# Optimization experiments

Hardware: AMD Instinct MI355X
Metric: run time of the kernel (lower is better)

## Reference

```python
import jax, jax.numpy as jnp
import numpy as np

N = 50000      # nodes
E = 800000     # edges per meta-path
P = 3          # meta-paths
IN = 128       # in_size
OUT = 64       # out_size per head
H = 4          # heads
HID = 128      # semantic-attention hidden
NEG_SLOPE = 0.2


def setup_inputs() -> dict:
    key = jax.random.key(0)
    ks = jax.random.split(key, 8)
    h = jax.random.normal(ks[0], (N, IN), jnp.float32)
    edges = jax.random.randint(ks[1], (P, 2, E), 0, N, dtype=jnp.int32)  # [P, (src,dst), E]
    fc_w = jax.random.normal(ks[2], (P, IN, H * OUT), jnp.float32) * 0.05
    attn_l = jax.random.normal(ks[3], (P, H, OUT), jnp.float32) * 0.05
    attn_r = jax.random.normal(ks[4], (P, H, OUT), jnp.float32) * 0.05
    w1 = jax.random.normal(ks[5], (H * OUT, HID), jnp.float32) * 0.05
    b1 = jnp.zeros((HID,), jnp.float32)
    w2 = jax.random.normal(ks[6], (HID,), jnp.float32) * 0.05
    return {"h": h, "edges": edges, "fc_w": fc_w, "attn_l": attn_l,
            "attn_r": attn_r, "w1": w1, "b1": b1, "w2": w2}


def _gat(h, edge, fc_w, al, ar):
    # One GATConv (DGL semantics, eval mode: dropout off, no residual/bias).
    src, dst = edge[0], edge[1]
    feat = (h @ fc_w).reshape(N, H, OUT)                 # [N,H,D]
    el = jnp.einsum('nhd,hd->nh', feat, al)              # [N,H]
    er = jnp.einsum('nhd,hd->nh', feat, ar)
    e = jax.nn.leaky_relu(el[src] + er[dst], NEG_SLOPE)  # [E,H]
    # edge softmax over incoming edges of each dst node
    m = jax.ops.segment_max(e, dst, num_segments=N)      # [N,H]
    m = jnp.where(jnp.isfinite(m), m, 0.0)               # empty segments -> 0
    ex = jnp.exp(e - m[dst])
    s = jax.ops.segment_sum(ex, dst, num_segments=N)     # [N,H]
    alpha = ex / s[dst]                                  # [E,H]
    msg = feat[src] * alpha[:, :, None]                  # [E,H,D]
    rst = jax.ops.segment_sum(msg, dst, num_segments=N)  # [N,H,D]
    return jax.nn.elu(rst).reshape(N, H * OUT)


def reference(h, edges, fc_w, attn_l, attn_r, w1, b1, w2):
    # per-meta-path GAT embeddings -> [N, P, H*OUT]
    z = jnp.stack([_gat(h, edges[i], fc_w[i], attn_l[i], attn_r[i])
                   for i in range(P)], axis=1)
    # semantic attention: Linear -> tanh -> Linear(no bias) -> softmax over P
    w = jnp.tanh(z @ w1 + b1) @ w2                       # [N,P]
    beta = jax.nn.softmax(w, axis=1)[:, :, None]         # [N,P,1]
    return (beta * z).sum(axis=1)                        # [N, H*OUT]
```

## Files before the change

kernel.cpp:

```cpp
#include <hip/hip_runtime.h>
#include <hip/hip_bf16.h>
#include <hip/hip_fp16.h>

#define N_NODES 50000
#define N_EDGES 800000
#define N_PATHS 3
#define IN_F    128
#define HO      256
#define N_HEADS 4
#define HID     128

#define BLK_PER_PATH 80
#define EDGES_PER_HB 10000
#define HIST_BLOCKS  (N_PATHS * BLK_PER_PATH)
#define PREP_BLOCKS  512
#define NPACK        12500
#define FEAT_RB      782
#define SCAT_BLOCKS  2344
#define FEAT_ELEMS   ((size_t)N_NODES * HO)

typedef __bf16 bf16;
typedef __bf16 bf16x8 __attribute__((ext_vector_type(8)));
typedef float  f32x4  __attribute__((ext_vector_type(4)));
typedef unsigned short u16;
typedef unsigned char  u8;
typedef unsigned int   u32;

__device__ __forceinline__ void prep_role(int b, const float* __restrict__ fc_w,
                                          const float* __restrict__ w1,
                                          bf16* __restrict__ fcwT,
                                          bf16* __restrict__ w1T) {
    int g = b * 256 + threadIdx.x;
    if (g < N_PATHS * IN_F * HO) {
        int p = g >> 15, r = g & 32767;
        int col = r & 255, k = r >> 8;
        fcwT[(size_t)p * 32768 + col * IN_F + k] = (bf16)fc_w[(size_t)p * 32768 + k * HO + col];
    } else {
        int gg = g - N_PATHS * IN_F * HO;
        if (gg < HO * HID) {
            int k = gg & 255, j = gg >> 8;
            w1T[(size_t)j * HO + k] = (bf16)w1[(size_t)k * HID + j];
        }
    }
}

__device__ __forceinline__ void hist_role(int b, const int* __restrict__ edges,
                                          u32* __restrict__ cnt32, u8* __restrict__ lrank,
                                          u32* hist) {
    const int p = b / BLK_PER_PATH, blk = b - p * BLK_PER_PATH;
    const int t = threadIdx.x;
    for (int i = t; i < NPACK; i += 256) hist[i] = 0;
    __syncthreads();

    const int* dstp = edges + (size_t)p * 2 * N_EDGES + N_EDGES + blk * EDGES_PER_HB;
    u8* lr = lrank + (size_t)p * N_EDGES + blk * EDGES_PER_HB;
    for (int q = t; q < EDGES_PER_HB / 4; q += 256) {
        int4 d4 = ((const int4*)dstp)[q];
        u32 o0 = atomicAdd(&hist[d4.x >> 2], 1u << ((d4.x & 3) * 8));
        u32 o1 = atomicAdd(&hist[d4.y >> 2], 1u << ((d4.y & 3) * 8));
        u32 o2 = atomicAdd(&hist[d4.z >> 2], 1u << ((d4.z & 3) * 8));
        u32 o3 = atomicAdd(&hist[d4.w >> 2], 1u << ((d4.w & 3) * 8));
        uchar4 r4;
        r4.x = (u8)(o0 >> ((d4.x & 3) * 8));
        r4.y = (u8)(o1 >> ((d4.y & 3) * 8));
        r4.z = (u8)(o2 >> ((d4.z & 3) * 8));
        r4.w = (u8)(o3 >> ((d4.w & 3) * 8));
        ((uchar4*)lr)[q] = r4;
    }
    __syncthreads();
    u32* out = cnt32 + (size_t)b * NPACK;
    for (int i = t; i < NPACK; i += 256) out[i] = hist[i];
}

__global__ __launch_bounds__(256) void k_ph(const float* __restrict__ fc_w,
                                            const float* __restrict__ w1,
                                            bf16* __restrict__ fcwT,
                                            bf16* __restrict__ w1T,
                                            const int* __restrict__ edges,
                                            u32* __restrict__ cnt32,
                                            u8* __restrict__ lrank) {
    __shared__ u32 hist[NPACK];
    const int bid = blockIdx.x;
    if (bid < PREP_BLOCKS)
        prep_role(bid, fc_w, w1, fcwT, w1T);
    else
        hist_role(bid - PREP_BLOCKS, edges, cnt32, lrank, hist);
}

__global__ __launch_bounds__(256) void k_base(u32* __restrict__ cnt32,
                                              int* __restrict__ deg) {
    int g = blockIdx.x * 256 + threadIdx.x;
    if (g >= N_PATHS * NPACK) return;
    int p = g / NPACK, q = g - p * NPACK;
    u32 s0 = 0, s1 = 0, s2 = 0, s3 = 0;
#pragma unroll 8
    for (int blk = 0; blk < BLK_PER_PATH; ++blk) {
        size_t idx = (size_t)(p * BLK_PER_PATH + blk) * NPACK + q;
        u32 c = cnt32[idx];
        cnt32[idx] = s0 | (s1 << 8) | (s2 << 16) | (s3 << 24);
        s0 += c & 0xff; s1 += (c >> 8) & 0xff; s2 += (c >> 16) & 0xff; s3 += c >> 24;
    }
    int4 d4 = {(int)s0, (int)s1, (int)s2, (int)s3};
    *(int4*)(deg + (size_t)p * N_NODES + 4 * q) = d4;
}

__global__ __launch_bounds__(1024) void k_scan(const int* __restrict__ deg,
                                               int* __restrict__ rowptr) {
    __shared__ int part[1024];
    const int p = blockIdx.x;
    const int* dg = deg + p * N_NODES;
    int* rp = rowptr + p * (N_NODES + 1);

    const int tid = threadIdx.x;
    const int CH = (N_NODES + 1023) / 1024;
    const int start = tid * CH;
    int s = 0;
    for (int i = 0; i < CH; ++i) { int idx = start + i; if (idx < N_NODES) s += dg[idx]; }
    part[tid] = s;
    __syncthreads();
    for (int off = 1; off < 1024; off <<= 1) {
        int v = (tid >= off) ? part[tid - off] : 0;
        __syncthreads();
        part[tid] += v;
        __syncthreads();
    }
    int excl = (tid == 0) ? 0 : part[tid - 1];
    for (int i = 0; i < CH; ++i) {
        int idx = start + i;
        if (idx < N_NODES) { rp[idx] = excl; excl += dg[idx]; }
    }
    if (tid == 1023) rp[N_NODES] = N_EDGES;
}

__device__ __forceinline__ void scatter_role(int b, const int* __restrict__ edges,
                                             const u8* __restrict__ lrank,
                                             const u32* __restrict__ cnt32,
                                             const int* __restrict__ rowptr,
                                             u16* __restrict__ csrAll) {
    int gt = b * 256 + threadIdx.x;
    if (gt >= (N_PATHS * N_EDGES) / 4) return;
    int base = gt * 4;
    int p = base / N_EDGES, e = base - p * N_EDGES;
    const int blk = e / EDGES_PER_HB;
    const int* ep = edges + (size_t)p * 2 * N_EDGES;
    int4 s4 = *(const int4*)(ep + e);
    int4 d4 = *(const int4*)(ep + N_EDGES + e);
    uchar4 r4 = *(const uchar4*)(lrank + base);
    const int* rp = rowptr + p * (N_NODES + 1);
    const u32* bb = cnt32 + (size_t)(p * BLK_PER_PATH + blk) * NPACK;
    u16* c = csrAll + (size_t)p * N_EDGES;
    int p0 = rp[d4.x] + (int)((bb[d4.x >> 2] >> ((d4.x & 3) * 8)) & 0xff) + r4.x;
    int p1 = rp[d4.y] + (int)((bb[d4.y >> 2] >> ((d4.y & 3) * 8)) & 0xff) + r4.y;
    int p2 = rp[d4.z] + (int)((bb[d4.z >> 2] >> ((d4.z & 3) * 8)) & 0xff) + r4.z;
    int p3 = rp[d4.w] + (int)((bb[d4.w >> 2] >> ((d4.w & 3) * 8)) & 0xff) + r4.w;
    c[p0] = (u16)s4.x; c[p1] = (u16)s4.y; c[p2] = (u16)s4.z; c[p3] = (u16)s4.w;
}

__device__ __forceinline__ void feat_role(int rb, const float* __restrict__ h,
                                          const bf16* __restrict__ fcwT,
                                          const float* __restrict__ al,
                                          const float* __restrict__ ar,
                                          __half* __restrict__ featAll,
                                          float* __restrict__ elAll,
                                          float* __restrict__ erAll) {
    const int t = threadIdx.x, w = t >> 6, l = t & 63, lo = l & 15, hi = l >> 4;
    const int arow = rb * 64 + w * 16 + lo;
    const int crow = rb * 64 + w * 16 + hi * 4;

    bf16x8 afr[4];
    if (arow < N_NODES) {
        const float* hp = h + (size_t)arow * IN_F;
#pragma unroll
        for (int ks = 0; ks < 4; ++ks) {
            float4 f0 = *(const float4*)(hp + ks * 32 + hi * 8);
            float4 f1 = *(const float4*)(hp + ks * 32 + hi * 8 + 4);
            bf16x8 a;
            a[0]=(bf16)f0.x; a[1]=(bf16)f0.y; a[2]=(bf16)f0.z; a[3]=(bf16)f0.w;
            a[4]=(bf16)f1.x; a[5]=(bf16)f1.y; a[6]=(bf16)f1.z; a[7]=(bf16)f1.w;
            afr[ks] = a;
        }
    } else {
#pragma unroll
        for (int ks = 0; ks < 4; ++ks) { bf16x8 a = {}; afr[ks] = a; }
    }

    for (int p = 0; p < N_PATHS; ++p) {
        __half* feat = featAll + (size_t)p * FEAT_ELEMS;
        const float* alp = al + p * HO;
        const float* arp = ar + p * HO;
        float* elA = elAll + (size_t)p * N_NODES * 4;
        float* erA = erAll + (size_t)p * N_NODES * 4;
#pragma unroll
        for (int ch = 0; ch < 2; ++ch) {
            const bf16* W = fcwT + (size_t)p * 32768 + (size_t)ch * 128 * IN_F;
            f32x4 acc[8];
#pragma unroll
            for (int c = 0; c < 8; ++c) { f32x4 zz = {0.f,0.f,0.f,0.f}; acc[c] = zz; }
#pragma unroll
            for (int ctl = 0; ctl < 8; ++ctl) {
                const bf16* wp = W + (size_t)(ctl * 16 + lo) * IN_F + hi * 8;
                f32x4 a = acc[ctl];
#pragma unroll
                for (int ks = 0; ks < 4; ++ks)
                    a = __builtin_amdgcn_mfma_f32_16x16x32_bf16(afr[ks], *(const bf16x8*)(wp + ks * 32), a, 0, 0, 0);
                acc[ctl] = a;
            }
            float elP[2][4] = {{0}}, erP[2][4] = {{0}};
#pragma unroll
            for (int ctl = 0; ctl < 8; ++ctl) {
                const int gcol = ch * 128 + ctl * 16 + lo;
                const float av = alp[gcol], bv = arp[gcol];
                const int hl = ctl >> 2;
#pragma unroll
                for (int rr = 0; rr < 4; ++rr) {
                    float v = acc[ctl][rr];
                    elP[hl][rr] = fmaf(v, av, elP[hl][rr]);
                    erP[hl][rr] = fmaf(v, bv, erP[hl][rr]);
                    if (crow + rr < N_NODES)
                        feat[(size_t)(crow + rr) * HO + gcol] = __float2half(v);
                }
            }
#pragma unroll
            for (int hl = 0; hl < 2; ++hl)
#pragma unroll
                for (int rr = 0; rr < 4; ++rr) {
                    float v = elP[hl][rr], u = erP[hl][rr];
#pragma unroll
                    for (int m = 1; m <= 8; m <<= 1) {
                        v += __shfl_xor(v, m, 64);
                        u += __shfl_xor(u, m, 64);
                    }
                    elP[hl][rr] = v; erP[hl][rr] = u;
                }
            if (lo == 0) {
#pragma unroll
                for (int rr = 0; rr < 4; ++rr) {
                    if (crow + rr < N_NODES) {
                        *(float2*)&elA[(crow + rr) * 4 + ch * 2] = make_float2(elP[0][rr], elP[1][rr]);
                        *(float2*)&erA[(crow + rr) * 4 + ch * 2] = make_float2(erP[0][rr], erP[1][rr]);
                    }
                }
            }
        }
    }
}

__global__ __launch_bounds__(256) void k_sf(const int* __restrict__ edges,
                                            const u8* __restrict__ lrank,
                                            const u32* __restrict__ cnt32,
                                            const int* __restrict__ rowptr,
                                            u16* __restrict__ csr,
                                            const float* __restrict__ h,
                                            const bf16* __restrict__ fcwT,
                                            const float* __restrict__ al,
                                            const float* __restrict__ ar,
                                            __half* __restrict__ featAll,
                                            float* __restrict__ elAll,
                                            float* __restrict__ erAll) {
    const int bid = blockIdx.x;
    if (bid < SCAT_BLOCKS)
        scatter_role(bid, edges, lrank, cnt32, rowptr, csr);
    else
        feat_role(bid - SCAT_BLOCKS, h, fcwT, al, ar, featAll, elAll, erAll);
}

__global__ __launch_bounds__(256) void k_gather3(const u16* __restrict__ csrAll,
                                                 const int* __restrict__ rowptrAll,
                                                 const float4* __restrict__ elAll,
                                                 const float4* __restrict__ erAll,
                                                 const __half* __restrict__ featAll,
                                                 bf16* __restrict__ z) {
    __shared__ u32     s_off[4][64];
    __shared__ __half2 s_ad[4][4][66];
    const int pb = blockIdx.x;
    const int p  = pb / (N_NODES / 4);
    const int nb = pb - p * (N_NODES / 4);

    const int t = threadIdx.x, w = t >> 6, l = t & 63;
    const int half = l >> 5, c = l & 31, hh = c >> 3;
    const int n = nb * 4 + w;

    const u16*    csr    = csrAll + (size_t)p * N_EDGES;
    const int*    rowptr = rowptrAll + p * (N_NODES + 1);
    const float4* el4    = elAll + (size_t)p * N_NODES;
    const __half* feat   = featAll + (size_t)p * FEAT_ELEMS;

    const int b0 = rowptr[n], b1e = rowptr[n + 1];
    const float4 er_n = (erAll + (size_t)p * N_NODES)[n];

    __half2 acc0 = __float2half2_rn(0.f), acc1 = acc0, acc2 = acc0, acc3 = acc0;
    float4 den = {0.f, 0.f, 0.f, 0.f};

    for (int base = b0; base < b1e; base += 64) {
        const int cnt = min(64, b1e - base);
        if (l < cnt) {
            int sv = csr[base + l];
            s_off[w][l] = (u32)(sv * HO);
            float4 e = el4[sv];
            float vx = e.x + er_n.x, vy = e.y + er_n.y,
                  vz = e.z + er_n.z, vw = e.w + er_n.w;
            vx = (vx >= 0.f) ? vx : 0.2f * vx;
            vy = (vy >= 0.f) ? vy : 0.2f * vy;
            vz = (vz >= 0.f) ? vz : 0.2f * vz;
            vw = (vw >= 0.f) ? vw : 0.2f * vw;
            float ex = __expf(vx), ey = __expf(vy), ez = __expf(vz), ew = __expf(vw);
            den.x += ex; den.y += ey; den.z += ez; den.w += ew;
            s_ad[w][0][l] = __float2half2_rn(ex);
            s_ad[w][1][l] = __float2half2_rn(ey);
            s_ad[w][2][l] = __float2half2_rn(ez);
            s_ad[w][3][l] = __float2half2_rn(ew);
        }
        int i2 = 0;
        for (; i2 + 8 <= cnt; i2 += 8) {
            const int e0 = i2 + half, e1 = i2 + 2 + half,
                      e2 = i2 + 4 + half, e3 = i2 + 6 + half;
            u32 o0 = s_off[w][e0], o1 = s_off[w][e1], o2 = s_off[w][e2], o3 = s_off[w][e3];
            __half2 a0 = s_ad[w][hh][e0], a1 = s_ad[w][hh][e1],
                    a2 = s_ad[w][hh][e2], a3 = s_ad[w][hh][e3];
            const uint4 u0 = *(const uint4*)(feat + o0 + c * 8);
            const uint4 u1 = *(const uint4*)(feat + o1 + c * 8);
            const uint4 u2 = *(const uint4*)(feat + o2 + c * 8);
            const uint4 u3 = *(const uint4*)(feat + o3 + c * 8);
            acc0 = __hfma2(__builtin_bit_cast(__half2, u0.x), a0, acc0);
            acc1 = __hfma2(__builtin_bit_cast(__half2, u0.y), a0, acc1);
            acc2 = __hfma2(__builtin_bit_cast(__half2, u0.z), a0, acc2);
            acc3 = __hfma2(__builtin_bit_cast(__half2, u0.w), a0, acc3);
            acc0 = __hfma2(__builtin_bit_cast(__half2, u1.x), a1, acc0);
            acc1 = __hfma2(__builtin_bit_cast(__half2, u1.y), a1, acc1);
            acc2 = __hfma2(__builtin_bit_cast(__half2, u1.z), a1, acc2);
            acc3 = __hfma2(__builtin_bit_cast(__half2, u1.w), a1, acc3);
            acc0 = __hfma2(__builtin_bit_cast(__half2, u2.x), a2, acc0);
            acc1 = __hfma2(__builtin_bit_cast(__half2, u2.y), a2, acc1);
            acc2 = __hfma2(__builtin_bit_cast(__half2, u2.z), a2, acc2);
            acc3 = __hfma2(__builtin_bit_cast(__half2, u2.w), a2, acc3);
            acc0 = __hfma2(__builtin_bit_cast(__half2, u3.x), a3, acc0);
            acc1 = __hfma2(__builtin_bit_cast(__half2, u3.y), a3, acc1);
            acc2 = __hfma2(__builtin_bit_cast(__half2, u3.z), a3, acc2);
            acc3 = __hfma2(__builtin_bit_cast(__half2, u3.w), a3, acc3);
        }
        for (; i2 + 4 <= cnt; i2 += 4) {
            const int e0 = i2 + half, e1 = i2 + 2 + half;
            u32 o0 = s_off[w][e0], o1 = s_off[w][e1];
            __half2 a0 = s_ad[w][hh][e0], a1 = s_ad[w][hh][e1];
            const uint4 u0 = *(const uint4*)(feat + o0 + c * 8);
            const uint4 u1 = *(const uint4*)(feat + o1 + c * 8);
            acc0 = __hfma2(__builtin_bit_cast(__half2, u0.x), a0, acc0);
            acc1 = __hfma2(__builtin_bit_cast(__half2, u0.y), a0, acc1);
            acc2 = __hfma2(__builtin_bit_cast(__half2, u0.z), a0, acc2);
            acc3 = __hfma2(__builtin_bit_cast(__half2, u0.w), a0, acc3);
            acc0 = __hfma2(__builtin_bit_cast(__half2, u1.x), a1, acc0);
            acc1 = __hfma2(__builtin_bit_cast(__half2, u1.y), a1, acc1);
            acc2 = __hfma2(__builtin_bit_cast(__half2, u1.z), a1, acc2);
            acc3 = __hfma2(__builtin_bit_cast(__half2, u1.w), a1, acc3);
        }
        for (; i2 < cnt; i2 += 2) {
            const int e = i2 + half;
            if (e < cnt) {
                u32 o0 = s_off[w][e];
                __half2 a0 = s_ad[w][hh][e];
                const uint4 u = *(const uint4*)(feat + o0 + c * 8);
                acc0 = __hfma2(__builtin_bit_cast(__half2, u.x), a0, acc0);
                acc1 = __hfma2(__builtin_bit_cast(__half2, u.y), a0, acc1);
                acc2 = __hfma2(__builtin_bit_cast(__half2, u.z), a0, acc2);
                acc3 = __hfma2(__builtin_bit_cast(__half2, u.w), a0, acc3);
            }
        }
    }

    float s[8];
    { float2 f0 = __half22float2(acc0), f1 = __half22float2(acc1),
             f2 = __half22float2(acc2), f3 = __half22float2(acc3);
      s[0]=f0.x; s[1]=f0.y; s[2]=f1.x; s[3]=f1.y; s[4]=f2.x; s[5]=f2.y; s[6]=f3.x; s[7]=f3.y; }
#pragma unroll
    for (int j = 0; j < 8; ++j) s[j] += __shfl_xor(s[j], 32, 64);
#pragma unroll
    for (int off = 32; off; off >>= 1) {
        den.x += __shfl_xor(den.x, off, 64);
        den.y += __shfl_xor(den.y, off, 64);
        den.z += __shfl_xor(den.z, off, 64);
        den.w += __shfl_xor(den.w, off, 64);
    }
    const float d = (hh == 0) ? den.x : (hh == 1) ? den.y : (hh == 2) ? den.z : den.w;
    const float inv = (d > 0.f) ? 1.f / d : 0.f;
    if (half == 0) {
        bf16x8 ov;
#pragma unroll
        for (int j = 0; j < 8; ++j) {
            float v = s[j] * inv;
            v = (v > 0.f) ? v : expm1f(v);
            ov[j] = (bf16)v;
        }
        *(bf16x8*)(z + (size_t)n * (N_PATHS * HO) + p * HO + c * 8) = ov;
    }
}

__global__ __launch_bounds__(256) void k_semout(const bf16* __restrict__ z,
                                                const bf16* __restrict__ w1T,
                                                const float* __restrict__ b1,
                                                const float* __restrict__ w2,
                                                float* __restrict__ out) {
    __shared__ bf16  zs[48 * 264];
    __shared__ float psem[4][48];
    __shared__ float betas[16][4];

    const int t = threadIdx.x, w = t >> 6, l = t & 63;
    const int lo = l & 15, hi = l >> 4;
    const int n0 = blockIdx.x * 16;

    bf16x8 bfr[2][8];
#pragma unroll
    for (int ct = 0; ct < 2; ++ct) {
        const int j = (2 * w + ct) * 16 + lo;
#pragma unroll
        for (int s = 0; s < 8; ++s)
            bfr[ct][s] = *(const bf16x8*)(w1T + (size_t)j * HO + s * 32 + hi * 8);
    }

    const uint4* zg4 = (const uint4*)(z + (size_t)n0 * (N_PATHS * HO));
    for (int i = t; i < 1536; i += 256) {
        uint4 v = zg4[i];
        int r = i >> 5, cin = (i & 31) * 8;
        *(uint4*)&zs[r * 264 + cin] = v;
    }
    __syncthreads();

    f32x4 acc[2][3];
#pragma unroll
    for (int ct = 0; ct < 2; ++ct)
#pragma unroll
        for (int m = 0; m < 3; ++m) { f32x4 zz = {0.f,0.f,0.f,0.f}; acc[ct][m] = zz; }

    for (int s = 0; s < 8; ++s) {
#pragma unroll
        for (int m = 0; m < 3; ++m) {
            bf16x8 a = *(const bf16x8*)&zs[(m * 16 + lo) * 264 + s * 32 + hi * 8];
            acc[0][m] = __builtin_amdgcn_mfma_f32_16x16x32_bf16(a, bfr[0][s], acc[0][m], 0, 0, 0);
            acc[1][m] = __builtin_amdgcn_mfma_f32_16x16x32_bf16(a, bfr[1][s], acc[1][m], 0, 0, 0);
        }
    }

    const int j0 = (2 * w + 0) * 16 + lo;
    const int j1 = (2 * w + 1) * 16 + lo;
    const float b1_0 = b1[j0], w2_0 = w2[j0];
    const float b1_1 = b1[j1], w2_1 = w2[j1];
#pragma unroll
    for (int m = 0; m < 3; ++m) {
#pragma unroll
        for (int r = 0; r < 4; ++r) {
            float tt = tanhf(acc[0][m][r] + b1_0) * w2_0
                     + tanhf(acc[1][m][r] + b1_1) * w2_1;
            tt += __shfl_xor(tt, 1, 64);
            tt += __shfl_xor(tt, 2, 64);
            tt += __shfl_xor(tt, 4, 64);
            tt += __shfl_xor(tt, 8, 64);
            if (lo == 0) psem[w][m * 16 + hi * 4 + r] = tt;
        }
    }
    __syncthreads();
    if (t < 48) psem[0][t] = psem[0][t] + psem[1][t] + psem[2][t] + psem[3][t];
    __syncthreads();
    if (t < 16) {
        float a0 = psem[0][3 * t], a1 = psem[0][3 * t + 1], a2 = psem[0][3 * t + 2];
        float mx = fmaxf(a0, fmaxf(a1, a2));
        float e0 = __expf(a0 - mx), e1 = __expf(a1 - mx), e2 = __expf(a2 - mx);
        float is = 1.f / (e0 + e1 + e2);
        betas[t][0] = e0 * is; betas[t][1] = e1 * is; betas[t][2] = e2 * is;
    }
    __syncthreads();
    for (int i = 0; i < 16; ++i) {
        float bb0 = betas[i][0], bb1 = betas[i][1], bb2 = betas[i][2];
        float o = bb0 * (float)zs[(3 * i + 0) * 264 + t]
                + bb1 * (float)zs[(3 * i + 1) * 264 + t]
                + bb2 * (float)zs[(3 * i + 2) * 264 + t];
        out[(size_t)(n0 + i) * HO + t] = o;
    }
}

static inline size_t align256(size_t x) { return (x + 255) & ~(size_t)255; }

extern "C" void kernel_launch(void* const* d_in, const int* in_sizes, int n_in,
                              void* d_out, int out_size, void* d_ws, size_t ws_size,
                              hipStream_t stream) {
    const float* h     = (const float*)d_in[0];
    const int*   edges = (const int*)d_in[1];
    const float* fc_w  = (const float*)d_in[2];
    const float* al    = (const float*)d_in[3];
    const float* ar    = (const float*)d_in[4];
    const float* w1    = (const float*)d_in[5];
    const float* b1    = (const float*)d_in[6];
    const float* w2    = (const float*)d_in[7];
    float* out = (float*)d_out;

    char* base = (char*)d_ws;
    size_t off = 0;
    auto carve = [&](size_t bytes) -> char* {
        char* p = base + off; off = align256(off + bytes); return p;
    };
    __half* feat   = (__half*)carve((size_t)N_PATHS * FEAT_ELEMS * 2);
    bf16*   zbuf   = (bf16*)carve((size_t)N_NODES * N_PATHS * HO * 2);
    u16*    csr    = (u16*)carve((size_t)N_PATHS * N_EDGES * 2);
    bf16*   fcwT   = (bf16*)carve((size_t)N_PATHS * IN_F * HO * 2);
    bf16*   w1T    = (bf16*)carve((size_t)HO * HID * 2);
    float*  el     = (float*)carve((size_t)N_PATHS * N_NODES * 4 * 4);
    float*  er     = (float*)carve((size_t)N_PATHS * N_NODES * 4 * 4);
    int*    deg    = (int*)carve((size_t)N_PATHS * N_NODES * 4);
    int*    rowptr = (int*)carve((size_t)N_PATHS * (N_NODES + 1) * 4);
    u8*     lrank  = (u8*)carve((size_t)N_PATHS * N_EDGES);
    u32*    cnt32  = (u32*)carve((size_t)HIST_BLOCKS * NPACK * 4);
    (void)ws_size; (void)in_sizes; (void)n_in; (void)out_size;

    k_ph<<<PREP_BLOCKS + HIST_BLOCKS, 256, 0, stream>>>(
        fc_w, w1, fcwT, w1T, edges, cnt32, lrank);
    k_base<<<(N_PATHS * NPACK + 255) / 256, 256, 0, stream>>>(cnt32, deg);
    k_scan<<<N_PATHS, 1024, 0, stream>>>(deg, rowptr);
    k_sf<<<SCAT_BLOCKS + FEAT_RB, 256, 0, stream>>>(
        edges, lrank, cnt32, rowptr, csr, h, fcwT, al, ar, feat, el, er);
    k_gather3<<<N_PATHS * (N_NODES / 4), 256, 0, stream>>>(
        csr, rowptr, (const float4*)el, (const float4*)er, feat, zbuf);
    k_semout<<<N_NODES / 16, 256, 0, stream>>>(zbuf, w1T, b1, w2, out);
}
```

Before: 487.6 us.

## Fuse degree scan into base kernel via last-block counter; pack gather LDS entries

Removes the separate k_scan launch. The last k_base block to finish, found through an atomic counter with thread fences, now runs the prefix scan for all three paths. That scan uses a single 256-thread block instead of three 1024-thread blocks, so it runs serially across paths with longer per-thread chunks. The gather kernel also packs each edge's source offset and half2 attention weight into one uint2 in shared memory, so each edge needs one LDS read instead of two.

```diff
diff --git a/kernel.cpp b/kernel.cpp
--- a/kernel.cpp
+++ b/kernel.cpp
@@ -17,6 +17,7 @@
 #define NPACK        12500
 #define FEAT_RB      782
 #define SCAT_BLOCKS  2344
+#define BASE_BLOCKS  147
 #define FEAT_ELEMS   ((size_t)N_NODES * HO)
 
 typedef __bf16 bf16;
@@ -29,7 +30,9 @@
 __device__ __forceinline__ void prep_role(int b, const float* __restrict__ fc_w,
                                           const float* __restrict__ w1,
                                           bf16* __restrict__ fcwT,
-                                          bf16* __restrict__ w1T) {
+                                          bf16* __restrict__ w1T,
+                                          u32* __restrict__ ctr) {
+    if (b == 0 && threadIdx.x == 0) *ctr = 0;
     int g = b * 256 + threadIdx.x;
     if (g < N_PATHS * IN_F * HO) {
         int p = g >> 15, r = g & 32767;
@@ -78,58 +81,68 @@
                                             bf16* __restrict__ w1T,
                                             const int* __restrict__ edges,
                                             u32* __restrict__ cnt32,
-                                            u8* __restrict__ lrank) {
+                                            u8* __restrict__ lrank,
+                                            u32* __restrict__ ctr) {
     __shared__ u32 hist[NPACK];
     const int bid = blockIdx.x;
     if (bid < PREP_BLOCKS)
-        prep_role(bid, fc_w, w1, fcwT, w1T);
+        prep_role(bid, fc_w, w1, fcwT, w1T, ctr);
     else
         hist_role(bid - PREP_BLOCKS, edges, cnt32, lrank, hist);
 }
 
 __global__ __launch_bounds__(256) void k_base(u32* __restrict__ cnt32,
-                                              int* __restrict__ deg) {
+                                              int* __restrict__ deg,
+                                              int* __restrict__ rowptr,
+                                              u32* __restrict__ ctr) {
     int g = blockIdx.x * 256 + threadIdx.x;
-    if (g >= N_PATHS * NPACK) return;
-    int p = g / NPACK, q = g - p * NPACK;
-    u32 s0 = 0, s1 = 0, s2 = 0, s3 = 0;
+    if (g < N_PATHS * NPACK) {
+        int p = g / NPACK, q = g - p * NPACK;
+        u32 s0 = 0, s1 = 0, s2 = 0, s3 = 0;
 #pragma unroll 8
-    for (int blk = 0; blk < BLK_PER_PATH; ++blk) {
-        size_t idx = (size_t)(p * BLK_PER_PATH + blk) * NPACK + q;
-        u32 c = cnt32[idx];
-        cnt32[idx] = s0 | (s1 << 8) | (s2 << 16) | (s3 << 24);
-        s0 += c & 0xff; s1 += (c >> 8) & 0xff; s2 += (c >> 16) & 0xff; s3 += c >> 24;
-    }
-    int4 d4 = {(int)s0, (int)s1, (int)s2, (int)s3};
-    *(int4*)(deg + (size_t)p * N_NODES + 4 * q) = d4;
-}
-
-__global__ __launch_bounds__(1024) void k_scan(const int* __restrict__ deg,
-                                               int* __restrict__ rowptr) {
-    __shared__ int part[1024];
-    const int p = blockIdx.x;
-    const int* dg = deg + p * N_NODES;
-    int* rp = rowptr + p * (N_NODES + 1);
-
+        for (int blk = 0; blk < BLK_PER_PATH; ++blk) {
+            size_t idx = (size_t)(p * BLK_PER_PATH + blk) * NPACK + q;
+            u32 c = cnt32[idx];
+            cnt32[idx] = s0 | (s1 << 8) | (s2 << 16) | (s3 << 24);
+            s0 += c & 0xff; s1 += (c >> 8) & 0xff; s2 += (c >> 16) & 0xff; s3 += c >> 24;
+        }
+        int4 d4 = {(int)s0, (int)s1, (int)s2, (int)s3};
+        *(int4*)(deg + (size_t)p * N_NODES + 4 * q) = d4;
+    }
+    __syncthreads();
+    __threadfence();
+    __shared__ u32 done;
+    if (threadIdx.x == 0) done = atomicAdd(ctr, 1);
+    __syncthreads();
+    if (done != (u32)(gridDim.x - 1)) return;
+    __threadfence();
+
+    __shared__ int part[256];
     const int tid = threadIdx.x;
-    const int CH = (N_NODES + 1023) / 1024;
-    const int start = tid * CH;
-    int s = 0;
-    for (int i = 0; i < CH; ++i) { int idx = start + i; if (idx < N_NODES) s += dg[idx]; }
-    part[tid] = s;
-    __syncthreads();
-    for (int off = 1; off < 1024; off <<= 1) {
-        int v = (tid >= off) ? part[tid - off] : 0;
+    const int CH = 196;
+    for (int p = 0; p < N_PATHS; ++p) {
+        const int* dg = deg + (size_t)p * N_NODES;
+        int* rp = rowptr + p * (N_NODES + 1);
+        const int st = tid * CH;
+        int s = 0;
+        for (int i = 0; i < CH; ++i) { int idx = st + i; if (idx < N_NODES) s += dg[idx]; }
+        part[tid] = s;
         __syncthreads();
-        part[tid] += v;
+        for (int off = 1; off < 256; off <<= 1) {
+            int v = (tid >= off) ? part[tid - off] : 0;
+            __syncthreads();
+            part[tid] += v;
+            __syncthreads();
+        }
+        int excl = (tid == 0) ? 0 : part[tid - 1];
+        for (int i = 0; i < CH; ++i) {
+            int idx = st + i;
+            if (idx < N_NODES) { rp[idx] = excl; excl += dg[idx]; }
+        }
+        if (tid == 255) rp[N_NODES] = N_EDGES;
         __syncthreads();
     }
-    int excl = (tid == 0) ? 0 : part[tid - 1];
-    for (int i = 0; i < CH; ++i) {
-        int idx = start + i;
-        if (idx < N_NODES) { rp[idx] = excl; excl += dg[idx]; }
-    }
-    if (tid == 1023) rp[N_NODES] = N_EDGES;
+    if (tid == 0) *ctr = 0;
 }
 
 __device__ __forceinline__ void scatter_role(int b, const int* __restrict__ edges,
@@ -270,8 +283,7 @@
                                                  const float4* __restrict__ erAll,
                                                  const __half* __restrict__ featAll,
                                                  bf16* __restrict__ z) {
-    __shared__ u32     s_off[4][64];
-    __shared__ __half2 s_ad[4][4][66];
+    __shared__ uint2 s_pk[4][4][66];
     const int pb = blockIdx.x;
     const int p  = pb / (N_NODES / 4);
     const int nb = pb - p * (N_NODES / 4);
@@ -295,7 +307,7 @@
         const int cnt = min(64, b1e - base);
         if (l < cnt) {
             int sv = csr[base + l];
-            s_off[w][l] = (u32)(sv * HO);
+            u32 off = (u32)(sv * HO);
             float4 e = el4[sv];
             float vx = e.x + er_n.x, vy = e.y + er_n.y,
                   vz = e.z + er_n.z, vw = e.w + er_n.w;
@@ -305,22 +317,30 @@
             vw = (vw >= 0.f) ? vw : 0.2f * vw;
             float ex = __expf(vx), ey = __expf(vy), ez = __expf(vz), ew = __expf(vw);
             den.x += ex; den.y += ey; den.z += ez; den.w += ew;
-            s_ad[w][0][l] = __float2half2_rn(ex);
-            s_ad[w][1][l] = __float2half2_rn(ey);
-            s_ad[w][2][l] = __float2half2_rn(ez);
-            s_ad[w][3][l] = __float2half2_rn(ew);
+            uint2 pk;
+            pk.x = off; pk.y = __builtin_bit_cast(u32, __float2half2_rn(ex));
+            s_pk[w][0][l] = pk;
+            pk.y = __builtin_bit_cast(u32, __float2half2_rn(ey));
+            s_pk[w][1][l] = pk;
+            pk.y = __builtin_bit_cast(u32, __float2half2_rn(ez));
+            s_pk[w][2][l] = pk;
+            pk.y = __builtin_bit_cast(u32, __float2half2_rn(ew));
+            s_pk[w][3][l] = pk;
         }
         int i2 = 0;
         for (; i2 + 8 <= cnt; i2 += 8) {
-            const int e0 = i2 + half, e1 = i2 + 2 + half,
-                      e2 = i2 + 4 + half, e3 = i2 + 6 + half;
-            u32 o0 = s_off[w][e0], o1 = s_off[w][e1], o2 = s_off[w][e2], o3 = s_off[w][e3];
-            __half2 a0 = s_ad[w][hh][e0], a1 = s_ad[w][hh][e1],
-                    a2 = s_ad[w][hh][e2], a3 = s_ad[w][hh][e3];
-            const uint4 u0 = *(const uint4*)(feat + o0 + c * 8);
-            const uint4 u1 = *(const uint4*)(feat + o1 + c * 8);
-            const uint4 u2 = *(const uint4*)(feat + o2 + c * 8);
-            const uint4 u3 = *(const uint4*)(feat + o3 + c * 8);
+            uint2 k0 = s_pk[w][hh][i2 + half];
+            uint2 k1 = s_pk[w][hh][i2 + 2 + half];
+            uint2 k2 = s_pk[w][hh][i2 + 4 + half];
+            uint2 k3 = s_pk[w][hh][i2 + 6 + half];
+            const uint4 u0 = *(const uint4*)(feat + k0.x + c * 8);
+            const uint4 u1 = *(const uint4*)(feat + k1.x + c * 8);
+            const uint4 u2 = *(const uint4*)(feat + k2.x + c * 8);
+            const uint4 u3 = *(const uint4*)(feat + k3.x + c * 8);
+            __half2 a0 = __builtin_bit_cast(__half2, k0.y);
+            __half2 a1 = __builtin_bit_cast(__half2, k1.y);
+            __half2 a2 = __builtin_bit_cast(__half2, k2.y);
+            __half2 a3 = __builtin_bit_cast(__half2, k3.y);
             acc0 = __hfma2(__builtin_bit_cast(__half2, u0.x), a0, acc0);
             acc1 = __hfma2(__builtin_bit_cast(__half2, u0.y), a0, acc1);
             acc2 = __hfma2(__builtin_bit_cast(__half2, u0.z), a0, acc2);
@@ -339,11 +359,12 @@
             acc3 = __hfma2(__builtin_bit_cast(__half2, u3.w), a3, acc3);
         }
         for (; i2 + 4 <= cnt; i2 += 4) {
-            const int e0 = i2 + half, e1 = i2 + 2 + half;
-            u32 o0 = s_off[w][e0], o1 = s_off[w][e1];
-            __half2 a0 = s_ad[w][hh][e0], a1 = s_ad[w][hh][e1];
-            const uint4 u0 = *(const uint4*)(feat + o0 + c * 8);
-            const uint4 u1 = *(const uint4*)(feat + o1 + c * 8);
+            uint2 k0 = s_pk[w][hh][i2 + half];
+            uint2 k1 = s_pk[w][hh][i2 + 2 + half];
+            const uint4 u0 = *(const uint4*)(feat + k0.x + c * 8);
+            const uint4 u1 = *(const uint4*)(feat + k1.x + c * 8);
+            __half2 a0 = __builtin_bit_cast(__half2, k0.y);
+            __half2 a1 = __builtin_bit_cast(__half2, k1.y);
             acc0 = __hfma2(__builtin_bit_cast(__half2, u0.x), a0, acc0);
             acc1 = __hfma2(__builtin_bit_cast(__half2, u0.y), a0, acc1);
             acc2 = __hfma2(__builtin_bit_cast(__half2, u0.z), a0, acc2);
@@ -356,9 +377,9 @@
         for (; i2 < cnt; i2 += 2) {
             const int e = i2 + half;
             if (e < cnt) {
-                u32 o0 = s_off[w][e];
-                __half2 a0 = s_ad[w][hh][e];
-                const uint4 u = *(const uint4*)(feat + o0 + c * 8);
+                uint2 k0 = s_pk[w][hh][e];
+                const uint4 u = *(const uint4*)(feat + k0.x + c * 8);
+                __half2 a0 = __builtin_bit_cast(__half2, k0.y);
                 acc0 = __hfma2(__builtin_bit_cast(__half2, u.x), a0, acc0);
                 acc1 = __hfma2(__builtin_bit_cast(__half2, u.y), a0, acc1);
                 acc2 = __hfma2(__builtin_bit_cast(__half2, u.z), a0, acc2);
@@ -507,12 +528,12 @@
     int*    rowptr = (int*)carve((size_t)N_PATHS * (N_NODES + 1) * 4);
     u8*     lrank  = (u8*)carve((size_t)N_PATHS * N_EDGES);
     u32*    cnt32  = (u32*)carve((size_t)HIST_BLOCKS * NPACK * 4);
+    u32*    ctr    = (u32*)carve(256);
     (void)ws_size; (void)in_sizes; (void)n_in; (void)out_size;
 
     k_ph<<<PREP_BLOCKS + HIST_BLOCKS, 256, 0, stream>>>(
-        fc_w, w1, fcwT, w1T, edges, cnt32, lrank);
-    k_base<<<(N_PATHS * NPACK + 255) / 256, 256, 0, stream>>>(cnt32, deg);
-    k_scan<<<N_PATHS, 1024, 0, stream>>>(deg, rowptr);
+        fc_w, w1, fcwT, w1T, edges, cnt32, lrank, ctr);
+    k_base<<<BASE_BLOCKS, 256, 0, stream>>>(cnt32, deg, rowptr, ctr);
     k_sf<<<SCAT_BLOCKS + FEAT_RB, 256, 0, stream>>>(
         edges, lrank, cnt32, rowptr, csr, h, fcwT, al, ar, feat, el, er);
     k_gather3<<<N_PATHS * (N_NODES / 4), 256, 0, stream>>>(
```

Result: slower. 699.8 us (+43.5%).

## Map one node per half-wave in gather kernel instead of one per wave

Applied to the files above, without the earlier changes.

The gather/aggregate kernel now assigns each 32-lane half of a wavefront its own destination node, with edge chunks of 32 staged in per-half shared memory. This removes the cross-half shuffle reduction of partial sums and the idle half during output writes, and halves the launch grid. In exchange, each half processes its node's edges serially, and degree imbalance between the two nodes sharing a wave can cause divergence.

```diff
diff --git a/kernel.cpp b/kernel.cpp
--- a/kernel.cpp
+++ b/kernel.cpp
@@ -270,15 +270,15 @@
                                                  const float4* __restrict__ erAll,
                                                  const __half* __restrict__ featAll,
                                                  bf16* __restrict__ z) {
-    __shared__ u32     s_off[4][64];
-    __shared__ __half2 s_ad[4][4][66];
+    __shared__ u32     s_off[4][2][32];
+    __shared__ __half2 s_ad[4][2][4][33];
     const int pb = blockIdx.x;
-    const int p  = pb / (N_NODES / 4);
-    const int nb = pb - p * (N_NODES / 4);
+    const int p  = pb / (N_NODES / 8);
+    const int nb = pb - p * (N_NODES / 8);
 
     const int t = threadIdx.x, w = t >> 6, l = t & 63;
-    const int half = l >> 5, c = l & 31, hh = c >> 3;
-    const int n = nb * 4 + w;
+    const int hf = l >> 5, c = l & 31, hh = c >> 3;
+    const int n = nb * 8 + w * 2 + hf;
 
     const u16*    csr    = csrAll + (size_t)p * N_EDGES;
     const int*    rowptr = rowptrAll + p * (N_NODES + 1);
@@ -291,11 +291,11 @@
     __half2 acc0 = __float2half2_rn(0.f), acc1 = acc0, acc2 = acc0, acc3 = acc0;
     float4 den = {0.f, 0.f, 0.f, 0.f};
 
-    for (int base = b0; base < b1e; base += 64) {
-        const int cnt = min(64, b1e - base);
-        if (l < cnt) {
-            int sv = csr[base + l];
-            s_off[w][l] = (u32)(sv * HO);
+    for (int base = b0; base < b1e; base += 32) {
+        const int cnt = min(32, b1e - base);
+        if (c < cnt) {
+            int sv = csr[base + c];
+            s_off[w][hf][c] = (u32)(sv * HO);
             float4 e = el4[sv];
             float vx = e.x + er_n.x, vy = e.y + er_n.y,
                   vz = e.z + er_n.z, vw = e.w + er_n.w;
@@ -305,18 +305,17 @@
             vw = (vw >= 0.f) ? vw : 0.2f * vw;
             float ex = __expf(vx), ey = __expf(vy), ez = __expf(vz), ew = __expf(vw);
             den.x += ex; den.y += ey; den.z += ez; den.w += ew;
-            s_ad[w][0][l] = __float2half2_rn(ex);
-            s_ad[w][1][l] = __float2half2_rn(ey);
-            s_ad[w][2][l] = __float2half2_rn(ez);
-            s_ad[w][3][l] = __float2half2_rn(ew);
-        }
-        int i2 = 0;
-        for (; i2 + 8 <= cnt; i2 += 8) {
-            const int e0 = i2 + half, e1 = i2 + 2 + half,
-                      e2 = i2 + 4 + half, e3 = i2 + 6 + half;
-            u32 o0 = s_off[w][e0], o1 = s_off[w][e1], o2 = s_off[w][e2], o3 = s_off[w][e3];
-            __half2 a0 = s_ad[w][hh][e0], a1 = s_ad[w][hh][e1],
-                    a2 = s_ad[w][hh][e2], a3 = s_ad[w][hh][e3];
+            s_ad[w][hf][0][c] = __float2half2_rn(ex);
+            s_ad[w][hf][1][c] = __float2half2_rn(ey);
+            s_ad[w][hf][2][c] = __float2half2_rn(ez);
+            s_ad[w][hf][3][c] = __float2half2_rn(ew);
+        }
+        int i = 0;
+        for (; i + 4 <= cnt; i += 4) {
+            u32 o0 = s_off[w][hf][i + 0], o1 = s_off[w][hf][i + 1];
+            u32 o2 = s_off[w][hf][i + 2], o3 = s_off[w][hf][i + 3];
+            __half2 a0 = s_ad[w][hf][hh][i + 0], a1 = s_ad[w][hf][hh][i + 1];
+            __half2 a2 = s_ad[w][hf][hh][i + 2], a3 = s_ad[w][hf][hh][i + 3];
             const uint4 u0 = *(const uint4*)(feat + o0 + c * 8);
             const uint4 u1 = *(const uint4*)(feat + o1 + c * 8);
             const uint4 u2 = *(const uint4*)(feat + o2 + c * 8);
@@ -338,43 +337,19 @@
             acc2 = __hfma2(__builtin_bit_cast(__half2, u3.z), a3, acc2);
             acc3 = __hfma2(__builtin_bit_cast(__half2, u3.w), a3, acc3);
         }
-        for (; i2 + 4 <= cnt; i2 += 4) {
-            const int e0 = i2 + half, e1 = i2 + 2 + half;
-            u32 o0 = s_off[w][e0], o1 = s_off[w][e1];
-            __half2 a0 = s_ad[w][hh][e0], a1 = s_ad[w][hh][e1];
-            const uint4 u0 = *(const uint4*)(feat + o0 + c * 8);
-            const uint4 u1 = *(const uint4*)(feat + o1 + c * 8);
-            acc0 = __hfma2(__builtin_bit_cast(__half2, u0.x), a0, acc0);
-            acc1 = __hfma2(__builtin_bit_cast(__half2, u0.y), a0, acc1);
-            acc2 = __hfma2(__builtin_bit_cast(__half2, u0.z), a0, acc2);
-            acc3 = __hfma2(__builtin_bit_cast(__half2, u0.w), a0, acc3);
-            acc0 = __hfma2(__builtin_bit_cast(__half2, u1.x), a1, acc0);
-            acc1 = __hfma2(__builtin_bit_cast(__half2, u1.y), a1, acc1);
-            acc2 = __hfma2(__builtin_bit_cast(__half2, u1.z), a1, acc2);
-            acc3 = __hfma2(__builtin_bit_cast(__half2, u1.w), a1, acc3);
-        }
-        for (; i2 < cnt; i2 += 2) {
-            const int e = i2 + half;
-            if (e < cnt) {
-                u32 o0 = s_off[w][e];
-                __half2 a0 = s_ad[w][hh][e];
-                const uint4 u = *(const uint4*)(feat + o0 + c * 8);
-                acc0 = __hfma2(__builtin_bit_cast(__half2, u.x), a0, acc0);
-                acc1 = __hfma2(__builtin_bit_cast(__half2, u.y), a0, acc1);
-                acc2 = __hfma2(__builtin_bit_cast(__half2, u.z), a0, acc2);
-                acc3 = __hfma2(__builtin_bit_cast(__half2, u.w), a0, acc3);
-            }
-        }
-    }
-
-    float s[8];
-    { float2 f0 = __half22float2(acc0), f1 = __half22float2(acc1),
-             f2 = __half22float2(acc2), f3 = __half22float2(acc3);
-      s[0]=f0.x; s[1]=f0.y; s[2]=f1.x; s[3]=f1.y; s[4]=f2.x; s[5]=f2.y; s[6]=f3.x; s[7]=f3.y; }
-#pragma unroll
-    for (int j = 0; j < 8; ++j) s[j] += __shfl_xor(s[j], 32, 64);
-#pragma unroll
-    for (int off = 32; off; off >>= 1) {
+        for (; i < cnt; ++i) {
+            u32 o0 = s_off[w][hf][i];
+            __half2 a0 = s_ad[w][hf][hh][i];
+            const uint4 u = *(const uint4*)(feat + o0 + c * 8);
+            acc0 = __hfma2(__builtin_bit_cast(__half2, u.x), a0, acc0);
+            acc1 = __hfma2(__builtin_bit_cast(__half2, u.y), a0, acc1);
+            acc2 = __hfma2(__builtin_bit_cast(__half2, u.z), a0, acc2);
+            acc3 = __hfma2(__builtin_bit_cast(__half2, u.w), a0, acc3);
+        }
+    }
+
+#pragma unroll
+    for (int off = 16; off; off >>= 1) {
         den.x += __shfl_xor(den.x, off, 64);
         den.y += __shfl_xor(den.y, off, 64);
         den.z += __shfl_xor(den.z, off, 64);
@@ -382,16 +357,18 @@
     }
     const float d = (hh == 0) ? den.x : (hh == 1) ? den.y : (hh == 2) ? den.z : den.w;
     const float inv = (d > 0.f) ? 1.f / d : 0.f;
-    if (half == 0) {
-        bf16x8 ov;
-#pragma unroll
-        for (int j = 0; j < 8; ++j) {
-            float v = s[j] * inv;
-            v = (v > 0.f) ? v : expm1f(v);
-            ov[j] = (bf16)v;
-        }
-        *(bf16x8*)(z + (size_t)n * (N_PATHS * HO) + p * HO + c * 8) = ov;
-    }
+
+    float2 f0 = __half22float2(acc0), f1 = __half22float2(acc1),
+           f2 = __half22float2(acc2), f3 = __half22float2(acc3);
+    float s[8] = {f0.x, f0.y, f1.x, f1.y, f2.x, f2.y, f3.x, f3.y};
+    bf16x8 ov;
+#pragma unroll
+    for (int j = 0; j < 8; ++j) {
+        float v = s[j] * inv;
+        v = (v > 0.f) ? v : expm1f(v);
+        ov[j] = (bf16)v;
+    }
+    *(bf16x8*)(z + (size_t)n * (N_PATHS * HO) + p * HO + c * 8) = ov;
 }
 
 __global__ __launch_bounds__(256) void k_semout(const bf16* __restrict__ z,
@@ -515,7 +492,7 @@
     k_scan<<<N_PATHS, 1024, 0, stream>>>(deg, rowptr);
     k_sf<<<SCAT_BLOCKS + FEAT_RB, 256, 0, stream>>>(
         edges, lrank, cnt32, rowptr, csr, h, fcwT, al, ar, feat, el, er);
-    k_gather3<<<N_PATHS * (N_NODES / 4), 256, 0, stream>>>(
+    k_gather3<<<N_PATHS * (N_NODES / 8), 256, 0, stream>>>(
         csr, rowptr, (const float4*)el, (const float4*)er, feat, zbuf);
     k_semout<<<N_NODES / 16, 256, 0, stream>>>(zbuf, w1T, b1, w2, out);
 }
```

After: 490.7 us. Within noise of the previous version (+0.6%).
